# Kernel tuning notes

Hardware: AMD Instinct MI355X
Metric: run time of the kernel (lower is better)

The kernel has to match this reference:

```python
import jax, jax.numpy as jnp
from jax import lax
import numpy as np

RADIUS = 0.1
NSAMPLE = 32
STRIDE = 3
ED_NSAMPLE = 10


def _sqdist(a, b):
    # a: [B,M,3], b: [B,N,3] -> [B,M,N] squared euclidean distance
    return (jnp.sum(a * a, -1)[:, :, None] + jnp.sum(b * b, -1)[:, None, :]
            - 2.0 * jnp.einsum('bmc,bnc->bmn', a, b))


def setup_inputs() -> dict:
    key = jax.random.key(0)
    ks = jax.random.split(key, 16)
    B, N = 8, 4096
    s = 0.05
    inp = {
        'data': jax.random.normal(ks[0], (B, N, 3), dtype=jnp.float32),
        'numpoints': N,
        # stem MLP 3 -> 64
        'W_stem': jax.random.normal(ks[1], (3, 64), dtype=jnp.float32) * s,
        'b_stem': jnp.zeros((64,), jnp.float32),
        # SA shared MLP (3 dp + 64 fj) -> 128
        'W_sa': jax.random.normal(ks[2], (67, 128), dtype=jnp.float32) * s,
        'b_sa': jnp.zeros((128,), jnp.float32),
        # FP MLP (128 interp + 64 skip) -> 64
        'W_fp': jax.random.normal(ks[3], (192, 64), dtype=jnp.float32) * s,
        'b_fp': jnp.zeros((64,), jnp.float32),
        # eigen-feature MLP 3 -> 4 -> 4
        'W_e1': jax.random.normal(ks[4], (3, 4), dtype=jnp.float32) * s,
        'b_e1': jnp.zeros((4,), jnp.float32),
        'W_e2': jax.random.normal(ks[5], (4, 4), dtype=jnp.float32) * s,
        'b_e2': jnp.zeros((4,), jnp.float32),
        # conv_final 1x1: 68 -> 64, + BN affine
        'W_fin': jax.random.normal(ks[6], (68, 64), dtype=jnp.float32) * s,
        'b_fin': jnp.zeros((64,), jnp.float32),
        'gamma': jnp.ones((64,), jnp.float32),
        'beta': jnp.zeros((64,), jnp.float32),
    }
    return inp


def reference(data, numpoints, W_stem, b_stem, W_sa, b_sa, W_fp, b_fp,
              W_e1, b_e1, W_e2, b_e2, W_fin, b_fin, gamma, beta):
    B, N, _ = data.shape
    b_ix = jnp.arange(B)[:, None, None]

    # ---------- encoder: stem MLP ----------
    f0 = jax.nn.relu(data @ W_stem + b_stem)  # [B,N,64]

    # set abstraction: stride-subsample centers, ball query, dp_fj, MLP, max
    sub_idx = jnp.arange(0, N, STRIDE)
    new_xyz = data[:, sub_idx]                 # [B,M,3]
    d2 = _sqdist(new_xyz, data)                # [B,M,N]
    col = jnp.arange(N, dtype=jnp.int32)
    valid = d2 < RADIUS * RADIUS
    keys = jnp.where(valid, col, N + col)      # first-valid ball query ordering
    negk, _ = lax.top_k(-keys, NSAMPLE)
    idx = -negk                                # [B,M,ns]
    first = idx[..., :1]                       # self point always valid
    idx = jnp.where(idx >= N, first, idx)
    g_xyz = data[b_ix, idx]                    # [B,M,ns,3]
    dp = (g_xyz - new_xyz[:, :, None, :]) / RADIUS  # normalize_dp
    g_f = f0[b_ix, idx]                        # [B,M,ns,64]
    feat = jnp.concatenate([dp, g_f], -1)      # [B,M,ns,67]
    h = jax.nn.relu(feat @ W_sa + b_sa)        # [B,M,ns,128]
    f_sub = jnp.max(h, axis=2)                 # [B,M,128]

    # ---------- decoder: 3-NN inverse-distance feature propagation ----------
    d2f = _sqdist(data, new_xyz)               # [B,N,M]
    negd, nn = lax.top_k(-d2f, 3)
    w = 1.0 / (-negd + 1e-8)
    w = w / jnp.sum(w, -1, keepdims=True)      # [B,N,3]
    nbr_f = f_sub[b_ix, nn]                    # [B,N,3,128]
    interp = jnp.einsum('bnk,bnkc->bnc', w, nbr_f)
    f = jax.nn.relu(jnp.concatenate([interp, f0], -1) @ W_fp + b_fp)  # [B,N,64]

    # ---------- KNN covariance eigen-features ----------
    d2e = _sqdist(data, data)                  # [B,N,N]
    _, gidx = lax.top_k(-d2e, ED_NSAMPLE)      # [B,N,k]
    nbr = data[b_ix, gidx]                     # [B,N,k,3]
    cen = nbr - jnp.mean(nbr, axis=2, keepdims=True)
    cov = jnp.einsum('bnkc,bnkd->bncd', cen, cen) / ED_NSAMPLE  # [B,N,3,3]
    eig = jnp.linalg.eigvalsh(cov)             # [B,N,3] ascending
    ef = jax.nn.relu(eig @ W_e1 + b_e1) @ W_e2 + b_e2  # [B,N,4]

    # ---------- fused 1x1 conv + BN (training-mode stats) + relu ----------
    z_in = jnp.concatenate([f, ef], -1)        # [B,N,68]
    zc = z_in @ W_fin + b_fin                  # [B,N,64]
    mu = jnp.mean(zc, axis=(0, 1))
    var = jnp.var(zc, axis=(0, 1))
    z = jax.nn.relu((zc - mu) * lax.rsqrt(var + 1e-5) * gamma + beta)
    z = jnp.transpose(z, (0, 2, 1))            # [B,64,N]
    return (data, z)
```

## Files before the change

### kernel.cpp

```cpp
#include <hip/hip_runtime.h>
#include <stdint.h>

#define BB 8
#define NN 4096
#define MM 1366
#define NS 32
#define RAD2 0.01f
#define NGRP 64
#define KW 8

__device__ __forceinline__ float rl(float v, int l) {
    return __int_as_float(__builtin_amdgcn_readlane(__float_as_int(v), l));
}
__device__ __forceinline__ uint32_t um(uint32_t a, uint32_t b) { return a < b ? a : b; }
__device__ __forceinline__ uint32_t ux(uint32_t a, uint32_t b) { return a > b ? a : b; }
__device__ __forceinline__ uint32_t um3(uint32_t a, uint32_t b, uint32_t c) { return um(um(a, b), c); }

__device__ __forceinline__ void mrg2(uint32_t* kk, uint32_t s0, uint32_t s1) {
    uint32_t n0 = um(kk[0], s0);
    uint32_t n1 = um3(kk[1], ux(kk[0], s0), s1);
    uint32_t n2 = um3(kk[2], ux(kk[1], s0), ux(kk[0], s1));
    uint32_t n3 = um3(kk[3], ux(kk[2], s0), ux(kk[1], s1));
    uint32_t n4 = um3(kk[4], ux(kk[3], s0), ux(kk[2], s1));
    uint32_t n5 = um3(kk[5], ux(kk[4], s0), ux(kk[3], s1));
    uint32_t n6 = um3(kk[6], ux(kk[5], s0), ux(kk[4], s1));
    uint32_t n7 = um3(kk[7], ux(kk[6], s0), ux(kk[5], s1));
    uint32_t n8 = um3(kk[8], ux(kk[7], s0), ux(kk[6], s1));
    uint32_t n9 = um3(kk[9], ux(kk[8], s0), ux(kk[7], s1));
    kk[0]=n0; kk[1]=n1; kk[2]=n2; kk[3]=n3; kk[4]=n4;
    kk[5]=n5; kk[6]=n6; kk[7]=n7; kk[8]=n8; kk[9]=n9;
}

__device__ __forceinline__ void mrg4(uint32_t* kk, uint32_t s0, uint32_t s1,
                                     uint32_t s2, uint32_t s3) {
    uint32_t n0 = um(kk[0], s0);
    uint32_t n1 = um3(kk[1], ux(kk[0], s0), s1);
    uint32_t n2 = um(um3(kk[2], ux(kk[1], s0), ux(kk[0], s1)), s2);
    uint32_t n3 = um3(um3(kk[3], ux(kk[2], s0), ux(kk[1], s1)), ux(kk[0], s2), s3);
    uint32_t n4 = um3(um3(kk[4], ux(kk[3], s0), ux(kk[2], s1)), ux(kk[1], s2), ux(kk[0], s3));
    uint32_t n5 = um3(um3(kk[5], ux(kk[4], s0), ux(kk[3], s1)), ux(kk[2], s2), ux(kk[1], s3));
    uint32_t n6 = um3(um3(kk[6], ux(kk[5], s0), ux(kk[4], s1)), ux(kk[3], s2), ux(kk[2], s3));
    uint32_t n7 = um3(um3(kk[7], ux(kk[6], s0), ux(kk[5], s1)), ux(kk[4], s2), ux(kk[3], s3));
    uint32_t n8 = um3(um3(kk[8], ux(kk[7], s0), ux(kk[6], s1)), ux(kk[5], s2), ux(kk[4], s3));
    uint32_t n9 = um3(um3(kk[9], ux(kk[8], s0), ux(kk[7], s1)), ux(kk[6], s2), ux(kk[5], s3));
    kk[0]=n0; kk[1]=n1; kk[2]=n2; kk[3]=n3; kk[4]=n4;
    kk[5]=n5; kk[6]=n6; kk[7]=n7; kk[8]=n8; kk[9]=n9;
}

__device__ __forceinline__ void srt4(uint32_t& a, uint32_t& b, uint32_t& c, uint32_t& d) {
    uint32_t t0 = um(a, b), t1 = ux(a, b), t2 = um(c, d), t3 = ux(c, d);
    uint32_t s0 = um(t0, t2), m0 = ux(t0, t2), m1 = um(t1, t3), s3 = ux(t1, t3);
    a = s0; b = um(m0, m1); c = ux(m0, m1); d = s3;
}

__device__ __forceinline__ uint32_t spr3(uint32_t v) {
    v = (v | (v << 4)) & 0xC3u;
    v = (v | (v << 2)) & 0x249u;
    return v;
}

__global__ __launch_bounds__(256) void k_stem(const float* __restrict__ data,
                                              const float* __restrict__ Ws,
                                              const float* __restrict__ bs,
                                              float* __restrict__ f0,
                                              float* __restrict__ out,
                                              float4* __restrict__ cand4) {
    int blk = blockIdx.x;
    if (blk >= (BB * NN * 64) / 256) {
        int t = (blk - (BB * NN * 64) / 256) * 256 + threadIdx.x;
        float x = data[t * 3], y = data[t * 3 + 1], z = data[t * 3 + 2];
        out[t * 3] = x; out[t * 3 + 1] = y; out[t * 3 + 2] = z;
        cand4[t] = make_float4(x, y, z, x * x + y * y + z * z);
        return;
    }
    int t = blk * 256 + threadIdx.x;
    int c = t & 63;
    int r = t >> 6;
    const float* d = data + r * 3;
    float acc = bs[c];
    acc = fmaf(d[0], Ws[c], acc);
    acc = fmaf(d[1], Ws[64 + c], acc);
    acc = fmaf(d[2], Ws[128 + c], acc);
    f0[t] = fmaxf(acc, 0.f);
}

__global__ __launch_bounds__(256) void k_sort(const float4* __restrict__ cand4,
                                              float4* __restrict__ cand4s,
                                              uint32_t* __restrict__ perm,
                                              float4* __restrict__ gbox) {
    __shared__ uint32_t cnt[4096];
    __shared__ uint32_t part[256];
    int b = blockIdx.x, t = threadIdx.x;
    const float4* cb = cand4 + b * NN;
    for (int i = t; i < 4096; i += 256) cnt[i] = 0;
    __syncthreads();
    uint32_t cid[16];
    #pragma unroll
    for (int u = 0; u < 16; ++u) {
        float4 c = cb[u * 256 + t];
        int ix = (int)floorf((c.x + 4.f) * 2.f);
        int iy = (int)floorf((c.y + 4.f) * 2.f);
        int iz = (int)floorf((c.z + 4.f) * 2.f);
        ix = ix < 0 ? 0 : (ix > 15 ? 15 : ix);
        iy = iy < 0 ? 0 : (iy > 15 ? 15 : iy);
        iz = iz < 0 ? 0 : (iz > 15 ? 15 : iz);
        uint32_t m = spr3((uint32_t)ix) | (spr3((uint32_t)iy) << 1) | (spr3((uint32_t)iz) << 2);
        cid[u] = m;
        atomicAdd(&cnt[m], 1u);
    }
    __syncthreads();
    uint32_t c16[16];
    uint32_t s = 0;
    #pragma unroll
    for (int u = 0; u < 16; ++u) { c16[u] = cnt[t * 16 + u]; s += c16[u]; }
    part[t] = s;
    __syncthreads();
    for (int off = 1; off < 256; off <<= 1) {
        uint32_t v = (t >= off) ? part[t - off] : 0u;
        __syncthreads();
        part[t] += v;
        __syncthreads();
    }
    uint32_t run = part[t] - s;
    #pragma unroll
    for (int u = 0; u < 16; ++u) { cnt[t * 16 + u] = run; run += c16[u]; }
    __syncthreads();
    #pragma unroll
    for (int u = 0; u < 16; ++u) {
        int p = u * 256 + t;
        uint32_t pos = atomicAdd(&cnt[cid[u]], 1u);
        cand4s[b * NN + pos] = cb[p];
        perm[b * NN + pos] = (uint32_t)p;
    }
    __syncthreads();
    if (t < NGRP) {
        float4 mn = make_float4(1e30f, 1e30f, 1e30f, 0.f);
        float4 mx = make_float4(-1e30f, -1e30f, -1e30f, 0.f);
        for (int j = 0; j < 64; ++j) {
            float4 c = cand4s[b * NN + t * 64 + j];
            mn.x = fminf(mn.x, c.x); mn.y = fminf(mn.y, c.y); mn.z = fminf(mn.z, c.z);
            mx.x = fmaxf(mx.x, c.x); mx.y = fmaxf(mx.y, c.y); mx.z = fmaxf(mx.z, c.z);
        }
        gbox[(b * NGRP + t) * 2]     = mn;
        gbox[(b * NGRP + t) * 2 + 1] = mx;
    }
}

__global__ __launch_bounds__(512) void k_knn(const float4* __restrict__ cand4s,
                                             const uint32_t* __restrict__ perm,
                                             const float4* __restrict__ gbox,
                                             uint32_t* __restrict__ mrg) {
    __shared__ float4 sBox[2 * NGRP];
    __shared__ uint32_t sKK[KW][64][10];
    __shared__ uint32_t sThr[64];
    __shared__ int sGrp[KW];
    __shared__ int sN;
    int t = threadIdx.x, w = t >> 6, lane = t & 63;
    int gw = blockIdx.x;
    int b = gw >> 6;
    int g = gw & (NGRP - 1);
    for (int i = t; i < 2 * NGRP; i += 512) sBox[i] = gbox[b * 2 * NGRP + i];
    __syncthreads();
    const float4* cs = cand4s + b * NN;
    const uint32_t* ps = perm + b * NN;
    float4 me = cs[g * 64 + lane];
    uint32_t mo = ps[g * 64 + lane];
    float px = me.x, py = me.y, pz = me.z, pa = me.w;
    uint32_t kk[10];
    #pragma unroll
    for (int r = 0; r < 10; ++r) kk[r] = 0xFFFFFF00u + r;

    auto scan_packets = [&](int jg, int j0, int j1, uint32_t thrC) {
        const float4* cp = cs + jg * 64;
        const uint4* pq = (const uint4*)(ps + jg * 64);
        uint32_t thr = um(kk[9], thrC);
        for (int j = j0; j < j1; ++j) {
            float4 ca  = cp[j * 4];
            float4 cbv = cp[j * 4 + 1];
            float4 cc  = cp[j * 4 + 2];
            float4 cd  = cp[j * 4 + 3];
            uint4 pm = pq[j];
            float da  = fmaxf(fmaf(-2.f, fmaf(pz, ca.z,  fmaf(py, ca.y,  px * ca.x)),  pa + ca.w),  0.f);
            float db_ = fmaxf(fmaf(-2.f, fmaf(pz, cbv.z, fmaf(py, cbv.y, px * cbv.x)), pa + cbv.w), 0.f);
            float dc  = fmaxf(fmaf(-2.f, fmaf(pz, cc.z,  fmaf(py, cc.y,  px * cc.x)),  pa + cc.w),  0.f);
            float dd  = fmaxf(fmaf(-2.f, fmaf(pz, cd.z,  fmaf(py, cd.y,  px * cd.x)),  pa + cd.w),  0.f);
            uint32_t ka = (__float_as_uint(da)  & 0xFFFFF000u) | pm.x;
            uint32_t kb = (__float_as_uint(db_) & 0xFFFFF000u) | pm.y;
            uint32_t kc = (__float_as_uint(dc)  & 0xFFFFF000u) | pm.z;
            uint32_t kd = (__float_as_uint(dd)  & 0xFFFFF000u) | pm.w;
            uint32_t mn4 = um(um(ka, kb), um(kc, kd));
            if (__ballot(mn4 < thr)) {
                srt4(ka, kb, kc, kd);
                mrg4(kk, ka, kb, kc, kd);
                thr = um(kk[9], thrC);
            }
        }
    };

    scan_packets(g, w * 2, w * 2 + 2, 0xFFFFFFFFu);

    float bdj = 1e30f;
    if (w == 0) {
        float4 amn = sBox[g * 2], amx = sBox[g * 2 + 1];
        float4 bmn = sBox[lane * 2], bmx = sBox[lane * 2 + 1];
        float bx = fmaxf(fmaxf(amn.x - bmx.x, bmn.x - amx.x), 0.f);
        float by = fmaxf(fmaxf(amn.y - bmx.y, bmn.y - amx.y), 0.f);
        float bz = fmaxf(fmaxf(amn.z - bmx.z, bmn.z - amx.z), 0.f);
        bdj = fmaf(bx, bx, fmaf(by, by, bz * bz));
        if (lane == g) bdj = 1e30f;
    }

    uint32_t tmp[10];
    for (int round = 0; round < 10; ++round) {
        #pragma unroll
        for (int r = 0; r < 10; ++r) sKK[w][lane][r] = kk[r];
        __syncthreads();
        if (w == 0) {
            #pragma unroll
            for (int r = 0; r < 10; ++r) tmp[r] = kk[r];
            for (int ww = 1; ww < KW; ++ww) {
                uint32_t s[10];
                #pragma unroll
                for (int r = 0; r < 10; ++r) s[r] = sKK[ww][lane][r];
                mrg4(tmp, s[0], s[1], s[2], s[3]);
                mrg4(tmp, s[4], s[5], s[6], s[7]);
                mrg2(tmp, s[8], s[9]);
            }
            sThr[lane] = tmp[9];
            uint32_t kb9 = tmp[9] & 0xFFFFF000u;
            float u2 = (kb9 >= 0x7F000000u) ? 1e30f : __uint_as_float(kb9 + 0x1000u);
            #pragma unroll
            for (int off = 1; off < 64; off <<= 1) u2 = fmaxf(u2, __shfl_xor(u2, off));
            float ubt = u2 * 1.0005f;
            int n = 0;
            #pragma unroll 1
            for (int s2 = 0; s2 < KW; ++s2) {
                float mind = bdj;
                #pragma unroll
                for (int off = 1; off < 64; off <<= 1) mind = fminf(mind, __shfl_xor(mind, off));
                if (!(mind < ubt)) break;
                unsigned long long mm2 = __ballot(bdj == mind);
                int jl = (int)__builtin_ctzll(mm2);
                if (lane == 0) sGrp[n] = jl;
                n++;
                if (lane == jl) bdj = 1e30f;
            }
            if (lane == 0) sN = n;
        }
        __syncthreads();
        int n = sN;
        if (n == 0) break;
        uint32_t thrC = sThr[lane];
        if (w == 0) { if (n == KW) scan_packets(sGrp[KW - 1], 0, 16, thrC); }
        else if (w - 1 < n) scan_packets(sGrp[w - 1], 0, 16, thrC);
    }
    if (w == 0) {
        int gp = b * NN + (int)mo;
        #pragma unroll
        for (int r = 0; r < 10; ++r) mrg[r * (BB * NN) + gp] = tmp[r];
    }
}

__device__ __forceinline__ void jrot(float& app, float& aqq, float& apq,
                                     float& arp, float& arq) {
    float ap = apq;
    if (fabsf(ap) > 1e-32f) {
        float th = (aqq - app) / (2.f * ap);
        float t = 1.f / (fabsf(th) + sqrtf(th * th + 1.f));
        t = th < 0.f ? -t : t;
        float c = 1.f / sqrtf(t * t + 1.f);
        float s = t * c;
        app = app - t * ap;
        aqq = aqq + t * ap;
        apq = 0.f;
        float rp = arp, rq = arq;
        arp = c * rp - s * rq;
        arq = s * rp + c * rq;
    }
}

__global__ __launch_bounds__(256) void k_knn_eig(const float4* __restrict__ cand4,
                                                 const uint32_t* __restrict__ mrg,
                                                 const float* __restrict__ We1,
                                                 const float* __restrict__ be1,
                                                 const float* __restrict__ We2,
                                                 const float* __restrict__ be2,
                                                 float* __restrict__ ef) {
    int t = blockIdx.x * 256 + threadIdx.x;
    int b = t >> 12;
    const float4* cb = cand4 + b * NN;
    uint32_t kk[10];
    #pragma unroll
    for (int r = 0; r < 10; ++r) kk[r] = mrg[r * (BB * NN) + t];
    float xs[10], ys[10], zs[10];
    float mx = 0.f, my = 0.f, mz = 0.f;
    #pragma unroll
    for (int r = 0; r < 10; ++r) {
        int n = (int)(kk[r] & 0xFFFu);
        float4 cr = cb[n];
        xs[r] = cr.x; ys[r] = cr.y; zs[r] = cr.z;
        mx += xs[r]; my += ys[r]; mz += zs[r];
    }
    mx *= 0.1f; my *= 0.1f; mz *= 0.1f;
    float a00 = 0, a01 = 0, a02 = 0, a11 = 0, a12 = 0, a22 = 0;
    #pragma unroll
    for (int r = 0; r < 10; ++r) {
        float x = xs[r] - mx, y = ys[r] - my, z = zs[r] - mz;
        a00 = fmaf(x, x, a00); a01 = fmaf(x, y, a01); a02 = fmaf(x, z, a02);
        a11 = fmaf(y, y, a11); a12 = fmaf(y, z, a12); a22 = fmaf(z, z, a22);
    }
    a00 *= 0.1f; a01 *= 0.1f; a02 *= 0.1f; a11 *= 0.1f; a12 *= 0.1f; a22 *= 0.1f;
    #pragma unroll
    for (int sweep = 0; sweep < 6; ++sweep) {
        jrot(a00, a11, a01, a02, a12);
        jrot(a00, a22, a02, a01, a12);
        jrot(a11, a22, a12, a01, a02);
    }
    float e0 = a00, e1 = a11, e2 = a22, tmp;
    if (e0 > e1) { tmp = e0; e0 = e1; e1 = tmp; }
    if (e1 > e2) { tmp = e1; e1 = e2; e2 = tmp; }
    if (e0 > e1) { tmp = e0; e0 = e1; e1 = tmp; }
    float tt[4];
    #pragma unroll
    for (int i = 0; i < 4; ++i) {
        float v = be1[i];
        v = fmaf(e0, We1[i], v);
        v = fmaf(e1, We1[4 + i], v);
        v = fmaf(e2, We1[8 + i], v);
        tt[i] = fmaxf(v, 0.f);
    }
    #pragma unroll
    for (int i = 0; i < 4; ++i) {
        float v = be2[i];
        v = fmaf(tt[0], We2[i], v);
        v = fmaf(tt[1], We2[4 + i], v);
        v = fmaf(tt[2], We2[8 + i], v);
        v = fmaf(tt[3], We2[12 + i], v);
        ef[t * 4 + i] = v;
    }
}

__global__ __launch_bounds__(256) void k_sa(const float4* __restrict__ cand4,
                                            const float* __restrict__ data,
                                            const float* __restrict__ f0,
                                            const uint32_t* __restrict__ mrg,
                                            const float* __restrict__ Wsa,
                                            const float* __restrict__ bsa,
                                            float* __restrict__ fsub) {
    __shared__ float2 sW[67 * 64];
    __shared__ int sIdx[4][NS];
    for (int i = threadIdx.x; i < 67 * 64; i += 256) {
        int k = i >> 6, c = i & 63;
        sW[i] = make_float2(Wsa[k * 128 + c], Wsa[k * 128 + 64 + c]);
    }
    __syncthreads();
    int wv = threadIdx.x >> 6, lane = threadIdx.x & 63;
    int gm = blockIdx.x * 4 + wv;
    if (gm >= BB * MM) return;
    int b = gm / MM, m = gm - b * MM;
    const float4* cb4 = cand4 + b * NN;
    const float* db = data + b * NN * 3;
    float4 cen = cb4[3 * m];
    float cx = cen.x, cy = cen.y, cz = cen.z, sa = cen.w;

    int cnt;
    bool fallback;
    {
        float d2l = 1e30f;
        int idxl = 0;
        if (lane < 10) {
            uint32_t key = mrg[lane * (BB * NN) + b * NN + 3 * m];
            idxl = (int)(key & 0xFFFu);
            float4 c = cb4[idxl];
            float dot = fmaf(cz, c.z, fmaf(cy, c.y, cx * c.x));
            d2l = (sa + c.w) - 2.f * dot;
        }
        bool valid = (lane < 10) && (d2l < RAD2);
        unsigned long long mask = __ballot(valid);
        if (valid) sIdx[wv][__popcll(mask & ((1ull << lane) - 1ull))] = idxl;
        cnt = __popcll(mask);
        fallback = rl(d2l, 9) < RAD2 * 1.0005f;
    }
    if (fallback) {
        cnt = 0;
        for (int base = 0; base < NN; base += 64) {
            int n = base + lane;
            float4 c = cb4[n];
            float dot = fmaf(cz, c.z, fmaf(cy, c.y, cx * c.x));
            float d2 = (sa + c.w) - 2.f * dot;
            bool valid = d2 < RAD2;
            unsigned long long mask = __ballot(valid);
            if (valid) {
                int pos = cnt + __popcll(mask & ((1ull << lane) - 1ull));
                if (pos < NS) sIdx[wv][pos] = n;
            }
            cnt += __popcll(mask);
            if (cnt >= NS) break;
        }
    }
    int scnt = cnt < NS ? cnt : NS;

    float cl = lane == 0 ? cx : (lane == 1 ? cy : cz);
    float hb0 = bsa[lane], hb1 = bsa[64 + lane];
    float m0 = 0.f, m1 = 0.f;

    for (int s0 = 0; s0 < scnt; s0 += 4) {
        float fr[4], fr2[4];
        #pragma unroll
        for (int u = 0; u < 4; ++u) {
            int s = s0 + u;
            if (s >= scnt) s = 0;
            int nj = sIdx[wv][s];
            int fb = (b * NN + nj) * 64;
            float v;
            if (lane >= 3) v = f0[fb + lane - 3];
            else           v = (db[nj * 3 + lane] - cl) * 10.0f;
            fr[u] = v;
            fr2[u] = (lane < 3) ? f0[fb + 61 + lane] : 0.f;
        }
        float h0[4], h1[4];
        #pragma unroll
        for (int u = 0; u < 4; ++u) { h0[u] = hb0; h1[u] = hb1; }
        for (int k = 0; k < 64; ++k) {
            float2 w = sW[k * 64 + lane];
            #pragma unroll
            for (int u = 0; u < 4; ++u) {
                float fv = rl(fr[u], k);
                h0[u] = fmaf(fv, w.x, h0[u]);
                h1[u] = fmaf(fv, w.y, h1[u]);
            }
        }
        #pragma unroll
        for (int k = 64; k < 67; ++k) {
            float2 w = sW[k * 64 + lane];
            #pragma unroll
            for (int u = 0; u < 4; ++u) {
                float fv = rl(fr2[u], k - 64);
                h0[u] = fmaf(fv, w.x, h0[u]);
                h1[u] = fmaf(fv, w.y, h1[u]);
            }
        }
        #pragma unroll
        for (int u = 0; u < 4; ++u) {
            m0 = fmaxf(m0, fmaxf(h0[u], 0.f));
            m1 = fmaxf(m1, fmaxf(h1[u], 0.f));
        }
    }
    fsub[gm * 128 + lane] = m0;
    fsub[gm * 128 + 64 + lane] = m1;
}

__global__ __launch_bounds__(512) void k_interp(const float4* __restrict__ cand4,
                                                const float* __restrict__ fsub,
                                                float* __restrict__ itp) {
    __shared__ float4 sC[MM];
    __shared__ float sMD[8][64][3];
    __shared__ int   sMI[8][64][3];
    __shared__ float sWts[64][3];
    __shared__ int   sNbr[64][3];
    int t = threadIdx.x, wv = t >> 6, lane = t & 63;
    int blk = blockIdx.x;
    int b = blk >> 6;
    int pbase = (blk & 63) * 64;
    const float4* cb4 = cand4 + b * NN;
    for (int m = t; m < MM; m += 512) sC[m] = cb4[3 * m];
    __syncthreads();
    int p = pbase + lane;
    float4 pm = cb4[p];
    float px = pm.x, py = pm.y, pz = pm.z, pa = pm.w;
    float d0 = 1e30f, d1 = 1e30f, d2v = 1e30f;
    int n0 = 0, n1 = 0, n2 = 0;
    int ms = wv * 171, me = ms + 171 < MM ? ms + 171 : MM;
    for (int m = ms; m < me; ++m) {
        float4 c = sC[m];
        float dd = (pa + c.w) - 2.f * (px * c.x + py * c.y + pz * c.z);
        if (dd < d2v) {
            if (dd < d1) {
                d2v = d1; n2 = n1;
                if (dd < d0) { d1 = d0; n1 = n0; d0 = dd; n0 = m; }
                else         { d1 = dd; n1 = m; }
            } else { d2v = dd; n2 = m; }
        }
    }
    sMD[wv][lane][0] = d0; sMD[wv][lane][1] = d1; sMD[wv][lane][2] = d2v;
    sMI[wv][lane][0] = n0; sMI[wv][lane][1] = n1; sMI[wv][lane][2] = n2;
    __syncthreads();
    if (wv == 0) {
        d0 = sMD[0][lane][0]; d1 = sMD[0][lane][1]; d2v = sMD[0][lane][2];
        n0 = sMI[0][lane][0]; n1 = sMI[0][lane][1]; n2 = sMI[0][lane][2];
        for (int w = 1; w < 8; ++w) {
            #pragma unroll
            for (int r = 0; r < 3; ++r) {
                float dd = sMD[w][lane][r];
                int mm = sMI[w][lane][r];
                if (dd < d2v) {
                    if (dd < d1) {
                        d2v = d1; n2 = n1;
                        if (dd < d0) { d1 = d0; n1 = n0; d0 = dd; n0 = mm; }
                        else         { d1 = dd; n1 = mm; }
                    } else { d2v = dd; n2 = mm; }
                }
            }
        }
        float w0 = 1.f / (d0 + 1e-8f), w1 = 1.f / (d1 + 1e-8f), w2 = 1.f / (d2v + 1e-8f);
        float ws = w0 + w1 + w2;
        sWts[lane][0] = w0 / ws; sWts[lane][1] = w1 / ws; sWts[lane][2] = w2 / ws;
        sNbr[lane][0] = n0; sNbr[lane][1] = n1; sNbr[lane][2] = n2;
    }
    __syncthreads();
    for (int i = wv * 8; i < wv * 8 + 8; ++i) {
        float a0 = sWts[i][0], a1 = sWts[i][1], a2 = sWts[i][2];
        const float* r0 = fsub + (b * MM + sNbr[i][0]) * 128;
        const float* r1 = fsub + (b * MM + sNbr[i][1]) * 128;
        const float* r2 = fsub + (b * MM + sNbr[i][2]) * 128;
        float v0 = fmaf(a2, r2[lane], fmaf(a1, r1[lane], a0 * r0[lane]));
        float v1 = fmaf(a2, r2[64 + lane], fmaf(a1, r1[64 + lane], a0 * r0[64 + lane]));
        int row = b * NN + pbase + i;
        itp[row * 128 + lane] = v0;
        itp[row * 128 + 64 + lane] = v1;
    }
}

__global__ __launch_bounds__(256) void k_fp(const float* __restrict__ itp,
                                            const float* __restrict__ f0,
                                            const float* __restrict__ W,
                                            const float* __restrict__ bias,
                                            float* __restrict__ outf) {
    __shared__ float sW[192 * 64];
    for (int i = threadIdx.x; i < 192 * 64; i += 256) sW[i] = W[i];
    __syncthreads();
    int lane = threadIdx.x & 63;
    int wv = threadIdx.x >> 6;
    float bb = bias[lane];
    int rowbase = blockIdx.x * 64 + wv * 16;
    for (int it = 0; it < 4; ++it) {
        int r = rowbase + it * 4;
        float fa[4], fbv[4], fc[4], acc[4];
        #pragma unroll
        for (int u = 0; u < 4; ++u) {
            fa[u]  = itp[(r + u) * 128 + lane];
            fbv[u] = itp[(r + u) * 128 + 64 + lane];
            fc[u]  = f0[(r + u) * 64 + lane];
            acc[u] = bb;
        }
        #pragma unroll
        for (int k = 0; k < 192; ++k) {
            float w = sW[k * 64 + lane];
            #pragma unroll
            for (int u = 0; u < 4; ++u) {
                float fv = k < 64 ? rl(fa[u], k)
                         : (k < 128 ? rl(fbv[u], k - 64) : rl(fc[u], k - 128));
                acc[u] = fmaf(fv, w, acc[u]);
            }
        }
        #pragma unroll
        for (int u = 0; u < 4; ++u)
            outf[(r + u) * 64 + lane] = fmaxf(acc[u], 0.f);
    }
}

__global__ __launch_bounds__(256) void k_fin(const float* __restrict__ fb,
                                             const float* __restrict__ efb,
                                             const float* __restrict__ W,
                                             const float* __restrict__ bias,
                                             float* __restrict__ zc) {
    __shared__ float sW[68 * 64];
    for (int i = threadIdx.x; i < 68 * 64; i += 256) sW[i] = W[i];
    __syncthreads();
    int lane = threadIdx.x & 63;
    int wv = threadIdx.x >> 6;
    float bb = bias[lane];
    int rowbase = blockIdx.x * 64 + wv * 16;
    for (int it = 0; it < 4; ++it) {
        int r = rowbase + it * 4;
        float fa[4], fe[4], acc[4];
        #pragma unroll
        for (int u = 0; u < 4; ++u) {
            fa[u] = fb[(r + u) * 64 + lane];
            fe[u] = (lane < 4) ? efb[(r + u) * 4 + lane] : 0.f;
            acc[u] = bb;
        }
        #pragma unroll
        for (int k = 0; k < 68; ++k) {
            float w = sW[k * 64 + lane];
            #pragma unroll
            for (int u = 0; u < 4; ++u) {
                float fv = k < 64 ? rl(fa[u], k) : rl(fe[u], k - 64);
                acc[u] = fmaf(fv, w, acc[u]);
            }
        }
        #pragma unroll
        for (int u = 0; u < 4; ++u)
            zc[(r + u) * 64 + lane] = acc[u];
    }
}

__global__ __launch_bounds__(256) void k_stats1(const float* __restrict__ zc,
                                                float* __restrict__ pp) {
    int t = threadIdx.x;
    int c = t & 63, r4 = t >> 6;
    float s = 0.f, sq = 0.f;
    int base = blockIdx.x * 512;
    for (int i = 0; i < 128; ++i) {
        float v = zc[(base + i * 4 + r4) * 64 + c];
        s += v;
        sq = fmaf(v, v, sq);
    }
    __shared__ float ls[256], lq[256];
    ls[t] = s; lq[t] = sq;
    __syncthreads();
    if (t < 64) {
        float st = ls[t] + ls[t + 64] + ls[t + 128] + ls[t + 192];
        float qt = lq[t] + lq[t + 64] + lq[t + 128] + lq[t + 192];
        pp[blockIdx.x * 128 + t] = st;
        pp[blockIdx.x * 128 + 64 + t] = qt;
    }
}

__global__ __launch_bounds__(64) void k_stats2(const float* __restrict__ pp,
                                               const float* __restrict__ gamma,
                                               const float* __restrict__ beta,
                                               float* __restrict__ ss) {
    int c = threadIdx.x;
    float s = 0.f, sq = 0.f;
    for (int k = 0; k < 64; ++k) {
        s += pp[k * 128 + c];
        sq += pp[k * 128 + 64 + c];
    }
    const float inv = 1.f / (float)(BB * NN);
    float mu = s * inv;
    float var = sq * inv - mu * mu;
    float sc = gamma[c] / sqrtf(var + 1e-5f);
    ss[c] = sc;
    ss[64 + c] = beta[c] - mu * sc;
}

__global__ __launch_bounds__(256) void k_norm_t(const float* __restrict__ zc,
                                                const float* __restrict__ ss,
                                                float* __restrict__ out) {
    __shared__ float sT[64][65];
    int blk = blockIdx.x;
    int b = blk >> 6;
    int nbase = (blk & 63) * 64;
    int c = threadIdx.x & 63;
    int r4 = threadIdx.x >> 6;
    float sc = ss[c], sh = ss[64 + c];
    #pragma unroll
    for (int i = 0; i < 16; ++i) {
        int nr = i * 4 + r4;
        float v = zc[(b * NN + nbase + nr) * 64 + c];
        sT[nr][c] = fmaxf(fmaf(v, sc, sh), 0.f);
    }
    __syncthreads();
    int nn = threadIdx.x & 63;
    #pragma unroll
    for (int i = 0; i < 16; ++i) {
        int cc = i * 4 + r4;
        out[BB * NN * 3 + (b * 64 + cc) * NN + nbase + nn] = sT[nn][cc];
    }
}

extern "C" void kernel_launch(void* const* d_in, const int* in_sizes, int n_in,
                              void* d_out, int out_size, void* d_ws, size_t ws_size,
                              hipStream_t stream) {
    const float* data = (const float*)d_in[0];
    const float* Wst  = (const float*)d_in[2];
    const float* bst  = (const float*)d_in[3];
    const float* Wsa  = (const float*)d_in[4];
    const float* bsa  = (const float*)d_in[5];
    const float* Wfp  = (const float*)d_in[6];
    const float* bfp  = (const float*)d_in[7];
    const float* We1  = (const float*)d_in[8];
    const float* be1  = (const float*)d_in[9];
    const float* We2  = (const float*)d_in[10];
    const float* be2  = (const float*)d_in[11];
    const float* Wfin = (const float*)d_in[12];
    const float* bfin = (const float*)d_in[13];
    const float* gamma = (const float*)d_in[14];
    const float* beta  = (const float*)d_in[15];
    float* out = (float*)d_out;

    float* f0   = (float*)d_ws;
    float* fsub = f0 + 2097152;
    float* efb  = fsub + 1398784;
    float* zc   = efb + 131072;
    float* ss   = zc + 2097152;
    float* pp   = ss + 128;
    float4* cand4 = (float4*)(pp + 8192);
    uint32_t* mrgb = (uint32_t*)((float*)cand4 + 131072);
    float* itp  = (float*)mrgb + 1310720;
    float* fb   = itp + 4194304;
    float4*   cand4s = (float4*)itp;
    uint32_t* perm   = (uint32_t*)(itp + 131072);
    float4*   gbox   = (float4*)(itp + 131072 + 32768);

    k_stem<<<(BB * NN * 64) / 256 + (BB * NN) / 256, 256, 0, stream>>>(
        data, Wst, bst, f0, out, cand4);
    k_sort<<<BB, 256, 0, stream>>>(cand4, cand4s, perm, gbox);
    k_knn<<<BB * NGRP, 512, 0, stream>>>(cand4s, perm, gbox, mrgb);
    k_knn_eig<<<(BB * NN) / 256, 256, 0, stream>>>(cand4, mrgb, We1, be1, We2, be2, efb);
    k_sa<<<(BB * MM + 3) / 4, 256, 0, stream>>>(cand4, data, f0, mrgb, Wsa, bsa, fsub);
    k_interp<<<BB * 64, 512, 0, stream>>>(cand4, fsub, itp);
    k_fp<<<512, 256, 0, stream>>>(itp, f0, Wfp, bfp, fb);
    k_fin<<<512, 256, 0, stream>>>(fb, efb, Wfin, bfin, zc);
    k_stats1<<<64, 256, 0, stream>>>(zc, pp);
    k_stats2<<<1, 64, 0, stream>>>(pp, gamma, beta, ss);
    k_norm_t<<<512, 256, 0, stream>>>(zc, ss, out);
}
```

Before: 341.4 us.

## Prefetch nearest 16 groups speculatively before cooperative KNN merge rounds

Every wave now computes box distances and orders the candidate groups redundantly, so no shared group list is needed. Before the first merge it scans the 8 nearest groups unconditionally, plus a second group when the box distance beats that wave's own bound. The later merge rounds let all 8 waves pick their own next group and prune using a shared threshold. This aims to cut the number of synchronized merge rounds and keep waves busy, but adds redundant reduction work per wave and may scan groups that turn out unnecessary.

```diff
diff --git a/kernel.cpp b/kernel.cpp
--- a/kernel.cpp
+++ b/kernel.cpp
@@ -153,7 +153,7 @@
     __shared__ float4 sBox[2 * NGRP];
     __shared__ uint32_t sKK[KW][64][10];
     __shared__ uint32_t sThr[64];
-    __shared__ int sGrp[KW];
+    __shared__ float sUb;
     __shared__ int sN;
     int t = threadIdx.x, w = t >> 6, lane = t & 63;
     int gw = blockIdx.x;
@@ -196,11 +196,16 @@
             }
         }
     };
-
-    scan_packets(g, w * 2, w * 2 + 2, 0xFFFFFFFFu);
-
-    float bdj = 1e30f;
-    if (w == 0) {
+    auto bound = [&]() {
+        uint32_t kb9 = kk[9] & 0xFFFFF000u;
+        float u2 = (kb9 >= 0x7F000000u) ? 1e30f : __uint_as_float(kb9 + 0x1000u);
+        #pragma unroll
+        for (int off = 1; off < 64; off <<= 1) u2 = fmaxf(u2, __shfl_xor(u2, off));
+        return u2;
+    };
+
+    float bdj;
+    {
         float4 amn = sBox[g * 2], amx = sBox[g * 2 + 1];
         float4 bmn = sBox[lane * 2], bmx = sBox[lane * 2 + 1];
         float bx = fmaxf(fmaxf(amn.x - bmx.x, bmn.x - amx.x), 0.f);
@@ -210,8 +215,27 @@
         if (lane == g) bdj = 1e30f;
     }
 
+    scan_packets(g, w * 2, w * 2 + 2, 0xFFFFFFFFu);
+
+    int g0 = 0, g1 = 0;
+    float bd1 = 1e30f;
+    for (int i = 0; i < 16; ++i) {
+        float mind = bdj;
+        #pragma unroll
+        for (int off = 1; off < 64; off <<= 1) mind = fminf(mind, __shfl_xor(mind, off));
+        unsigned long long mm = __ballot(bdj == mind);
+        int jl = (int)__builtin_ctzll(mm);
+        if (i == w) g0 = jl;
+        if (i == w + 8) { g1 = jl; bd1 = mind; }
+        if (lane == jl) bdj = 1e30f;
+    }
+    scan_packets(g0, 0, 16, 0xFFFFFFFFu);
+    if (bd1 < bound() * 1.0005f)
+        scan_packets(g1, 0, 16, 0xFFFFFFFFu);
+
+    int rb = 16;
     uint32_t tmp[10];
-    for (int round = 0; round < 10; ++round) {
+    while (true) {
         #pragma unroll
         for (int r = 0; r < 10; ++r) sKK[w][lane][r] = kk[r];
         __syncthreads();
@@ -232,27 +256,32 @@
             #pragma unroll
             for (int off = 1; off < 64; off <<= 1) u2 = fmaxf(u2, __shfl_xor(u2, off));
             float ubt = u2 * 1.0005f;
+            float mind = bdj;
+            #pragma unroll
+            for (int off = 1; off < 64; off <<= 1) mind = fminf(mind, __shfl_xor(mind, off));
             int n = 0;
-            #pragma unroll 1
-            for (int s2 = 0; s2 < KW; ++s2) {
-                float mind = bdj;
-                #pragma unroll
-                for (int off = 1; off < 64; off <<= 1) mind = fminf(mind, __shfl_xor(mind, off));
-                if (!(mind < ubt)) break;
-                unsigned long long mm2 = __ballot(bdj == mind);
-                int jl = (int)__builtin_ctzll(mm2);
-                if (lane == 0) sGrp[n] = jl;
-                n++;
-                if (lane == jl) bdj = 1e30f;
-            }
-            if (lane == 0) sN = n;
+            if (rb < NGRP - 1 && mind < ubt)
+                n = (NGRP - 1 - rb) < KW ? (NGRP - 1 - rb) : KW;
+            if (lane == 0) { sN = n; sUb = ubt; }
         }
         __syncthreads();
         int n = sN;
         if (n == 0) break;
+        float ubt = sUb;
         uint32_t thrC = sThr[lane];
-        if (w == 0) { if (n == KW) scan_packets(sGrp[KW - 1], 0, 16, thrC); }
-        else if (w - 1 < n) scan_packets(sGrp[w - 1], 0, 16, thrC);
+        int eg = -1; float ebd = 1e30f;
+        for (int i = 0; i < n; ++i) {
+            float mind = bdj;
+            #pragma unroll
+            for (int off = 1; off < 64; off <<= 1) mind = fminf(mind, __shfl_xor(mind, off));
+            unsigned long long mm = __ballot(bdj == mind);
+            int jl = (int)__builtin_ctzll(mm);
+            if (i == w) { eg = jl; ebd = mind; }
+            if (lane == jl) bdj = 1e30f;
+        }
+        if (w < n && ebd < ubt)
+            scan_packets(eg, 0, 16, thrC);
+        rb += n;
     }
     if (w == 0) {
         int gp = b * NN + (int)mo;
```

Measured after the change: 342.7 us. About the same (+0.4%).
